# Kernel tuning notes

Measured on AMD Instinct MI355X. Metric: run time of the kernel, lower is better.

Reference implementation:

```python
import jax, jax.numpy as jnp
import numpy as np

N_PTS = 100000
C_IN, C_OUT, K = 16, 32, 3
B, D, H, W = 2, 32, 128, 128


def setup_inputs() -> dict:
    key = jax.random.key(0)
    kf, kw, kb, kz, ky, kx = jax.random.split(key, 6)
    features = jax.random.normal(kf, (N_PTS, C_IN), dtype=jnp.float32)
    coords = jnp.stack([
        jax.random.randint(kb, (N_PTS,), 0, B),
        jax.random.randint(kz, (N_PTS,), 0, D),
        jax.random.randint(ky, (N_PTS,), 0, H),
        jax.random.randint(kx, (N_PTS,), 0, W),
    ], axis=1).astype(jnp.int32)
    weight = jax.random.normal(kw, (K ** 3, C_IN, C_OUT), dtype=jnp.float32) * 0.01
    bias = jnp.zeros((C_OUT,), dtype=jnp.float32)
    return {"features": features, "coords": coords, "weight": weight, "bias": bias,
            "batch_size": B, "d_sp": D, "h_sp": H, "w_sp": W}


def reference(features, coords, weight, bias, batch_size, d_sp, h_sp, w_sp):
    # Scatter sparse voxel features into dense grid (B, C_in, D, H, W).
    n, c_in = features.shape
    c_out = weight.shape[2]
    k = K
    b, z, y, x = coords[:, 0], coords[:, 1], coords[:, 2], coords[:, 3]
    dense = jnp.zeros((batch_size, c_in, d_sp, h_sp, w_sp), dtype=features.dtype)
    dense = dense.at[b, :, z, y, x].set(features)  # (N,) advanced idx -> rows of (N, C_in)
    # Conv3d: torch copies weight.view(C_out, C_in, k, k, k) -> OIDHW kernel.
    kernel = weight.reshape(c_out, c_in, k, k, k)
    out = jax.lax.conv_general_dilated(
        dense, kernel,
        window_strides=(1, 1, 1),
        padding=[(1, 1), (1, 1), (1, 1)],
        dimension_numbers=("NCDHW", "OIDHW", "NCDHW"))
    out = jax.nn.relu(out + bias[None, :, None, None, None])
    # Dense equivalent of the torch nonzero-gather (which has data-dependent
    # shape): return the full dense activated grid (B, C_out, D, H, W).
    return out
```

## Files before the change

### kernel.cpp

```cpp
#include <hip/hip_runtime.h>

#define CIN   16
#define COUT  32
#define BATCH 2
#define DSP   32
#define HSP   128
#define WSP   128
#define NVOX  (BATCH*DSP*HSP*WSP)

#define DP (DSP+2)
#define HP (HSP+2)
#define WP (WSP+2)
#define ZSTR (HP*WP)
#define NVOXP (BATCH*DP*HP*WP)
#define NDCH  (NVOXP*2)

#define TZ 4
#define TY 8
#define TX 32
#define PZ 6
#define PYY 10
#define PXX 34
#define PROW (PYY*PXX)
#define PVOX (PZ*PROW)
#define NCHUNK (2*PVOX)
#define NCHPAD 4096
#define NPAIR 14
#define NWREP ((NPAIR*2*64*8 + 255)/256)

typedef __bf16 bf16x8 __attribute__((ext_vector_type(8)));
typedef float  f32x4  __attribute__((ext_vector_type(4)));

__device__ __forceinline__ void load_lds16(const void* g, void* l) {
    __builtin_amdgcn_global_load_lds(
        (const __attribute__((address_space(1))) unsigned*)g,
        (__attribute__((address_space(3))) unsigned*)l, 16, 0, 0);
}

__global__ void k_prep(const int4* __restrict__ coords, int n, int nbDedup,
                       int* __restrict__ map,
                       const float* __restrict__ w, __bf16* __restrict__ wpack) {
    int bb = blockIdx.x;
    if (bb < nbDedup) {
        int p = bb * 256 + threadIdx.x;
        if (p >= n) return;
        int4 c = coords[p];
        int vox = ((c.x*DSP + c.y)*HSP + c.z)*WSP + c.w;
        atomicMax(&map[vox], p);
    } else {
        int i = (bb - nbDedup) * 256 + threadIdx.x;
        if (i >= NPAIR*2*64*8) return;
        int j = i & 7, l = (i>>3) & 63, h = (i>>9) & 1, p = i >> 10;
        int tap = 2*p + ((l>>4)>>1);
        int co  = h*16 + (l & 15);
        int ci  = ((l>>4)&1)*8 + j;
        float v = (tap < 27) ? w[(co*CIN + ci)*27 + tap] : 0.0f;
        wpack[i] = (__bf16)v;
    }
}

__global__ void k_fill(const int* __restrict__ map, const float* __restrict__ feat,
                       __bf16* __restrict__ dense) {
    int c = blockIdx.x * 256 + threadIdx.x;
    if (c >= NDCH) return;
    int v = c >> 1, h = c & 1;
    int bb = v / (DP*ZSTR);
    int r  = v - bb*(DP*ZSTR);
    int zp = r / ZSTR;  r -= zp*ZSTR;
    int yp = r / WP;
    int xp = r - yp*WP;
    bf16x8 val = { (__bf16)0.f,(__bf16)0.f,(__bf16)0.f,(__bf16)0.f,
                   (__bf16)0.f,(__bf16)0.f,(__bf16)0.f,(__bf16)0.f };
    if ((unsigned)(zp-1) < DSP && (unsigned)(yp-1) < HSP && (unsigned)(xp-1) < WSP) {
        int vox = ((bb*DSP + (zp-1))*HSP + (yp-1))*WSP + (xp-1);
        int p = map[vox];
        if (p >= 0) {
            const float4* fp = (const float4*)(feat + (size_t)p*CIN) + h*2;
            float4 f0 = fp[0], f1 = fp[1];
            val = bf16x8{ (__bf16)f0.x,(__bf16)f0.y,(__bf16)f0.z,(__bf16)f0.w,
                          (__bf16)f1.x,(__bf16)f1.y,(__bf16)f1.z,(__bf16)f1.w };
        }
    }
    *(bf16x8*)(dense + (size_t)v*CIN + h*8) = val;
}

__device__ __forceinline__ void stage_tile(const __bf16* __restrict__ gb,
                                           ushort* lbase, int wave, int lane) {
    #pragma unroll
    for (int it = 0; it < 8; ++it) {
        int j0 = wave*64 + it*512;
        int j  = j0 + lane;
        int jj = j < NCHUNK ? j : NCHUNK-1;
        int h  = (jj >= PVOX) ? 1 : 0;
        int v  = jj - h*PVOX;
        int pz = v / PROW;
        int rem = v - pz*PROW;
        int py = rem / PXX;
        int px = rem - py*PXX;
        load_lds16(gb + ((size_t)(pz*ZSTR + py*WP + px))*CIN + h*8,
                   (void*)(lbase + (size_t)j0*8));
    }
}

__global__ __launch_bounds__(512, 2) void k_conv(
    const __bf16* __restrict__ dense, const __bf16* __restrict__ wpack,
    const float* __restrict__ bias, float* __restrict__ out)
{
    __shared__ __align__(16) ushort patch[2][NCHPAD*8];

    int bid = blockIdx.x;
    int bs  = (bid & 7) * 32 + (bid >> 3);
    int tyi = bs & 15, tzi = (bs >> 4) & 7, b = bs >> 7;
    int z0 = tzi*TZ, y0 = tyi*TY;

    int tid  = threadIdx.x;
    int lane = tid & 63, wave = tid >> 6;
    int lx16  = lane & 15;
    int lhalf = (lane >> 4) & 1;
    int ltp   = (lane >> 4) >> 1;
    int zw    = wave >> 1;
    int yb    = (wave & 1) * 4;

    int voff[NPAIR];
    #pragma unroll
    for (int p = 0; p < NPAIR; ++p) {
        int tap = 2*p + ltp; if (tap > 26) tap = 26;
        int kd = tap/9, kh = (tap/3)%3, kw = tap%3;
        voff[p] = (kd*PYY + kh)*PXX + kw;
    }
    float bv0 = bias[lx16], bv1 = bias[16 + lx16];

    bf16x8 wf[NPAIR][2];
    #pragma unroll
    for (int p = 0; p < NPAIR; ++p)
        #pragma unroll
        for (int h = 0; h < 2; ++h)
            wf[p][h] = *(const bf16x8*)(wpack + (size_t)((p*2 + h)*64 + lane)*8);

    const __bf16* grow = dense + ((((size_t)b*DP + z0)*HP + y0)*WP)*CIN;

    stage_tile(grow, patch[0], wave, lane);

    #pragma unroll 1
    for (int t = 0; t < 4; ++t) {
        if (t < 3) stage_tile(grow + (size_t)(t+1)*TX*CIN, patch[(t+1)&1], wave, lane);
        if (t == 0)      asm volatile("s_waitcnt vmcnt(8)\ns_barrier"  ::: "memory");
        else if (t < 3)  asm volatile("s_waitcnt vmcnt(24)\ns_barrier" ::: "memory");
        else             asm volatile("s_waitcnt vmcnt(16)\ns_barrier" ::: "memory");
        __builtin_amdgcn_sched_barrier(0);

        f32x4 acc[8][2];
        #pragma unroll
        for (int gi = 0; gi < 8; ++gi) {
            acc[gi][0] = (f32x4){0.f,0.f,0.f,0.f};
            acc[gi][1] = (f32x4){0.f,0.f,0.f,0.f};
        }
        const ushort* pb = patch[t&1] +
            ((size_t)lhalf*PVOX + (zw*PYY + yb)*PXX + lx16)*8;
        #pragma unroll
        for (int p = 0; p < NPAIR; ++p) {
            const ushort* pa = pb + (size_t)voff[p]*8;
            #pragma unroll
            for (int gi = 0; gi < 8; ++gi) {
                bf16x8 a = *(const bf16x8*)(pa + ((gi>>1)*PXX + (gi&1)*16)*8);
                acc[gi][0] = __builtin_amdgcn_mfma_f32_16x16x32_bf16(a, wf[p][0], acc[gi][0], 0,0,0);
                acc[gi][1] = __builtin_amdgcn_mfma_f32_16x16x32_bf16(a, wf[p][1], acc[gi][1], 0,0,0);
            }
        }

        asm volatile("s_barrier" ::: "memory");
        __builtin_amdgcn_sched_barrier(0);

        #pragma unroll
        for (int gi = 0; gi < 8; ++gi) {
            int y = yb + (gi >> 1), xg = gi & 1;
            int gz = z0 + zw, gy = y0 + y;
            int gx = t*TX + xg*16 + ((lane >> 4) << 2);
            f32x4 o0, o1;
            o0[0] = fmaxf(acc[gi][0][0]+bv0, 0.f); o0[1] = fmaxf(acc[gi][0][1]+bv0, 0.f);
            o0[2] = fmaxf(acc[gi][0][2]+bv0, 0.f); o0[3] = fmaxf(acc[gi][0][3]+bv0, 0.f);
            o1[0] = fmaxf(acc[gi][1][0]+bv1, 0.f); o1[1] = fmaxf(acc[gi][1][1]+bv1, 0.f);
            o1[2] = fmaxf(acc[gi][1][2]+bv1, 0.f); o1[3] = fmaxf(acc[gi][1][3]+bv1, 0.f);
            size_t base0 = ((((size_t)b*COUT + lx16)*DSP + gz)*HSP + gy)*WSP + gx;
            size_t base1 = base0 + (size_t)16*DSP*HSP*WSP;
            *(f32x4*)(out + base0) = o0;
            *(f32x4*)(out + base1) = o1;
        }
    }
}

extern "C" void kernel_launch(void* const* d_in, const int* in_sizes, int n_in,
                              void* d_out, int out_size, void* d_ws, size_t ws_size,
                              hipStream_t stream) {
    const float* feat   = (const float*)d_in[0];
    const int4*  coords = (const int4*)d_in[1];
    const float* weight = (const float*)d_in[2];
    const float* bias   = (const float*)d_in[3];
    float* out = (float*)d_out;
    int n = in_sizes[0] / CIN;

    int*    map   = (int*)d_ws;
    __bf16* dense = (__bf16*)(map + NVOX);
    __bf16* wpack = dense + (size_t)NVOXP*CIN;

    hipMemsetAsync(map, 0xFF, (size_t)NVOX*sizeof(int), stream);

    int nb = (n + 255) / 256;
    k_prep<<<nb + NWREP, 256, 0, stream>>>(coords, n, nb, map, weight, wpack);
    k_fill<<<(NDCH + 255)/256, 256, 0, stream>>>(map, feat, dense);
    k_conv<<<256, 512, 0, stream>>>(dense, wpack, bias, out);
}
```

Baseline: 73.41 us.

## Switch conv to 16x16x16 MFMA with channel-quartered layout and z-register reuse

The dense grid is re-laid out as four channel-quarter planes of 4 bf16 each, and the conv uses 16x16x16 bf16 MFMAs per tap instead of tap-paired 16x16x32. Each wave now owns one y row across all 4 z slices. It loads 6 z-planes of patch data once per (kh,kw,xg) and reuses them across the kd taps, which cuts LDS reads. The trade-off is twice as many MFMA instructions, each doing half the work, plus 27 weight fragments held in registers and more complex fill-kernel indexing.

```diff
diff --git a/kernel.cpp b/kernel.cpp
--- a/kernel.cpp
+++ b/kernel.cpp
@@ -11,9 +11,8 @@
 #define DP (DSP+2)
 #define HP (HSP+2)
 #define WP (WSP+2)
-#define ZSTR (HP*WP)
 #define NVOXP (BATCH*DP*HP*WP)
-#define NDCH  (NVOXP*2)
+#define NDCH2 (BATCH*4*DP*HP*(WP/2))
 
 #define TZ 4
 #define TY 8
@@ -23,13 +22,26 @@
 #define PXX 34
 #define PROW (PYY*PXX)
 #define PVOX (PZ*PROW)
-#define NCHUNK (2*PVOX)
+#define QCH   (PVOX/2)
+#define QUSH  (PVOX*4)
+#define NCHUNK (4*QCH)
 #define NCHPAD 4096
-#define NPAIR 14
-#define NWREP ((NPAIR*2*64*8 + 255)/256)
-
-typedef __bf16 bf16x8 __attribute__((ext_vector_type(8)));
+#define NWREP ((27*2*64*4 + 255)/256)
+
+typedef __bf16 bf16x4 __attribute__((ext_vector_type(4)));
+typedef short  s16x4  __attribute__((ext_vector_type(4)));
 typedef float  f32x4  __attribute__((ext_vector_type(4)));
+
+#if defined(__HIP_DEVICE_COMPILE__)
+  #if __has_builtin(__builtin_amdgcn_mfma_f32_16x16x16bf16_1k)
+    #define MFMA16(A,B,C) __builtin_amdgcn_mfma_f32_16x16x16bf16_1k((A),(B),(C),0,0,0)
+  #else
+    #define MFMA16(A,B,C) __builtin_amdgcn_mfma_f32_16x16x16_bf16( \
+        __builtin_bit_cast(bf16x4,(A)), __builtin_bit_cast(bf16x4,(B)), (C),0,0,0)
+  #endif
+#else
+  #define MFMA16(A,B,C) (C)
+#endif
 
 __device__ __forceinline__ void load_lds16(const void* g, void* l) {
     __builtin_amdgcn_global_load_lds(
@@ -49,39 +61,40 @@
         atomicMax(&map[vox], p);
     } else {
         int i = (bb - nbDedup) * 256 + threadIdx.x;
-        if (i >= NPAIR*2*64*8) return;
-        int j = i & 7, l = (i>>3) & 63, h = (i>>9) & 1, p = i >> 10;
-        int tap = 2*p + ((l>>4)>>1);
-        int co  = h*16 + (l & 15);
-        int ci  = ((l>>4)&1)*8 + j;
-        float v = (tap < 27) ? w[(co*CIN + ci)*27 + tap] : 0.0f;
-        wpack[i] = (__bf16)v;
+        if (i >= 27*2*64*4) return;
+        int j = i & 3, l = (i>>2) & 63, h = (i>>8) & 1, tap = i >> 9;
+        int co = h*16 + (l & 15);
+        int ci = (l>>4)*4 + j;
+        wpack[i] = (__bf16)w[(co*CIN + ci)*27 + tap];
     }
 }
 
 __global__ void k_fill(const int* __restrict__ map, const float* __restrict__ feat,
-                       __bf16* __restrict__ dense) {
+                       __bf16* __restrict__ dense2) {
     int c = blockIdx.x * 256 + threadIdx.x;
-    if (c >= NDCH) return;
-    int v = c >> 1, h = c & 1;
-    int bb = v / (DP*ZSTR);
-    int r  = v - bb*(DP*ZSTR);
-    int zp = r / ZSTR;  r -= zp*ZSTR;
-    int yp = r / WP;
-    int xp = r - yp*WP;
-    bf16x8 val = { (__bf16)0.f,(__bf16)0.f,(__bf16)0.f,(__bf16)0.f,
-                   (__bf16)0.f,(__bf16)0.f,(__bf16)0.f,(__bf16)0.f };
-    if ((unsigned)(zp-1) < DSP && (unsigned)(yp-1) < HSP && (unsigned)(xp-1) < WSP) {
-        int vox = ((bb*DSP + (zp-1))*HSP + (yp-1))*WSP + (xp-1);
-        int p = map[vox];
-        if (p >= 0) {
-            const float4* fp = (const float4*)(feat + (size_t)p*CIN) + h*2;
-            float4 f0 = fp[0], f1 = fp[1];
-            val = bf16x8{ (__bf16)f0.x,(__bf16)f0.y,(__bf16)f0.z,(__bf16)f0.w,
-                          (__bf16)f1.x,(__bf16)f1.y,(__bf16)f1.z,(__bf16)f1.w };
+    if (c >= NDCH2) return;
+    int px2 = c % 65;  int r1 = c / 65;
+    int yp  = r1 % HP; int r2 = r1 / HP;
+    int zp  = r2 % DP; int r3 = r2 / DP;
+    int q   = r3 & 3;  int b  = r3 >> 2;
+    ushort out8[8] = {0,0,0,0,0,0,0,0};
+    if ((unsigned)(zp-1) < DSP && (unsigned)(yp-1) < HSP) {
+        #pragma unroll
+        for (int s = 0; s < 2; ++s) {
+            int gx = 2*px2 + s - 1;
+            if ((unsigned)gx < WSP) {
+                int vox = ((b*DSP + (zp-1))*HSP + (yp-1))*WSP + gx;
+                int p = map[vox];
+                if (p >= 0) {
+                    float4 f = *(const float4*)(feat + (size_t)p*CIN + q*4);
+                    bf16x4 v = { (__bf16)f.x, (__bf16)f.y, (__bf16)f.z, (__bf16)f.w };
+                    *(bf16x4*)&out8[s*4] = v;
+                }
+            }
         }
     }
-    *(bf16x8*)(dense + (size_t)v*CIN + h*8) = val;
+    size_t idx = ((((size_t)(b*4 + q)*DP + zp)*HP + yp)*WP + 2*px2)*4;
+    *(uint4*)(dense2 + idx) = *(uint4*)out8;
 }
 
 __device__ __forceinline__ void stage_tile(const __bf16* __restrict__ gb,
@@ -91,19 +104,20 @@
         int j0 = wave*64 + it*512;
         int j  = j0 + lane;
         int jj = j < NCHUNK ? j : NCHUNK-1;
-        int h  = (jj >= PVOX) ? 1 : 0;
-        int v  = jj - h*PVOX;
+        int q  = jj / QCH;
+        int c2 = jj - q*QCH;
+        int v  = c2*2;
         int pz = v / PROW;
         int rem = v - pz*PROW;
         int py = rem / PXX;
         int px = rem - py*PXX;
-        load_lds16(gb + ((size_t)(pz*ZSTR + py*WP + px))*CIN + h*8,
+        load_lds16(gb + ((size_t)q*DP*HP*WP + (size_t)pz*HP*WP + (size_t)py*WP + px)*4,
                    (void*)(lbase + (size_t)j0*8));
     }
 }
 
 __global__ __launch_bounds__(512, 2) void k_conv(
-    const __bf16* __restrict__ dense, const __bf16* __restrict__ wpack,
+    const __bf16* __restrict__ dense2, const __bf16* __restrict__ wpack,
     const float* __restrict__ bias, float* __restrict__ out)
 {
     __shared__ __align__(16) ushort patch[2][NCHPAD*8];
@@ -115,72 +129,74 @@
 
     int tid  = threadIdx.x;
     int lane = tid & 63, wave = tid >> 6;
-    int lx16  = lane & 15;
-    int lhalf = (lane >> 4) & 1;
-    int ltp   = (lane >> 4) >> 1;
-    int zw    = wave >> 1;
-    int yb    = (wave & 1) * 4;
-
-    int voff[NPAIR];
+    int lx16 = lane & 15;
+    int lq   = lane >> 4;
+
+    float bv0 = bias[lx16], bv1 = bias[16 + lx16];
+
+    s16x4 wf[27][2];
     #pragma unroll
-    for (int p = 0; p < NPAIR; ++p) {
-        int tap = 2*p + ltp; if (tap > 26) tap = 26;
-        int kd = tap/9, kh = (tap/3)%3, kw = tap%3;
-        voff[p] = (kd*PYY + kh)*PXX + kw;
-    }
-    float bv0 = bias[lx16], bv1 = bias[16 + lx16];
-
-    bf16x8 wf[NPAIR][2];
-    #pragma unroll
-    for (int p = 0; p < NPAIR; ++p)
+    for (int tap = 0; tap < 27; ++tap)
         #pragma unroll
         for (int h = 0; h < 2; ++h)
-            wf[p][h] = *(const bf16x8*)(wpack + (size_t)((p*2 + h)*64 + lane)*8);
-
-    const __bf16* grow = dense + ((((size_t)b*DP + z0)*HP + y0)*WP)*CIN;
+            wf[tap][h] = *(const s16x4*)(wpack + (size_t)((tap*2 + h)*64 + lane)*4);
+
+    const __bf16* grow = dense2 + (((size_t)(b*4)*DP + z0)*HP + y0)*(size_t)WP*4;
 
     stage_tile(grow, patch[0], wave, lane);
 
     #pragma unroll 1
     for (int t = 0; t < 4; ++t) {
-        if (t < 3) stage_tile(grow + (size_t)(t+1)*TX*CIN, patch[(t+1)&1], wave, lane);
+        if (t < 3) stage_tile(grow + (size_t)(t+1)*TX*4, patch[(t+1)&1], wave, lane);
         if (t == 0)      asm volatile("s_waitcnt vmcnt(8)\ns_barrier"  ::: "memory");
         else if (t < 3)  asm volatile("s_waitcnt vmcnt(24)\ns_barrier" ::: "memory");
         else             asm volatile("s_waitcnt vmcnt(16)\ns_barrier" ::: "memory");
         __builtin_amdgcn_sched_barrier(0);
 
-        f32x4 acc[8][2];
-        #pragma unroll
-        for (int gi = 0; gi < 8; ++gi) {
-            acc[gi][0] = (f32x4){0.f,0.f,0.f,0.f};
-            acc[gi][1] = (f32x4){0.f,0.f,0.f,0.f};
-        }
-        const ushort* pb = patch[t&1] +
-            ((size_t)lhalf*PVOX + (zw*PYY + yb)*PXX + lx16)*8;
-        #pragma unroll
-        for (int p = 0; p < NPAIR; ++p) {
-            const ushort* pa = pb + (size_t)voff[p]*8;
+        f32x4 acc[4][2][2];
+        #pragma unroll
+        for (int z = 0; z < 4; ++z)
             #pragma unroll
-            for (int gi = 0; gi < 8; ++gi) {
-                bf16x8 a = *(const bf16x8*)(pa + ((gi>>1)*PXX + (gi&1)*16)*8);
-                acc[gi][0] = __builtin_amdgcn_mfma_f32_16x16x32_bf16(a, wf[p][0], acc[gi][0], 0,0,0);
-                acc[gi][1] = __builtin_amdgcn_mfma_f32_16x16x32_bf16(a, wf[p][1], acc[gi][1], 0,0,0);
+            for (int xg = 0; xg < 2; ++xg) {
+                acc[z][xg][0] = (f32x4){0.f,0.f,0.f,0.f};
+                acc[z][xg][1] = (f32x4){0.f,0.f,0.f,0.f};
             }
+        const ushort* pbase = patch[t&1] + lq*QUSH;
+        #pragma unroll
+        for (int kh = 0; kh < 3; ++kh)
+        #pragma unroll
+        for (int kw = 0; kw < 3; ++kw)
+        #pragma unroll
+        for (int xg = 0; xg < 2; ++xg) {
+            int vbase = (wave + kh)*PXX + xg*16 + kw + lx16;
+            s16x4 r[6];
+            #pragma unroll
+            for (int pz = 0; pz < 6; ++pz)
+                r[pz] = *(const s16x4*)(pbase + (size_t)(pz*PROW + vbase)*4);
+            #pragma unroll
+            for (int z = 0; z < 4; ++z)
+                #pragma unroll
+                for (int kd = 0; kd < 3; ++kd) {
+                    int tap = (kd*3 + kh)*3 + kw;
+                    acc[z][xg][0] = MFMA16(r[z+kd], wf[tap][0], acc[z][xg][0]);
+                    acc[z][xg][1] = MFMA16(r[z+kd], wf[tap][1], acc[z][xg][1]);
+                }
         }
 
         asm volatile("s_barrier" ::: "memory");
         __builtin_amdgcn_sched_barrier(0);
 
         #pragma unroll
-        for (int gi = 0; gi < 8; ++gi) {
-            int y = yb + (gi >> 1), xg = gi & 1;
-            int gz = z0 + zw, gy = y0 + y;
-            int gx = t*TX + xg*16 + ((lane >> 4) << 2);
+        for (int z = 0; z < 4; ++z)
+        #pragma unroll
+        for (int xg = 0; xg < 2; ++xg) {
+            int gz = z0 + z, gy = y0 + wave;
+            int gx = t*TX + xg*16 + (lq << 2);
             f32x4 o0, o1;
-            o0[0] = fmaxf(acc[gi][0][0]+bv0, 0.f); o0[1] = fmaxf(acc[gi][0][1]+bv0, 0.f);
-            o0[2] = fmaxf(acc[gi][0][2]+bv0, 0.f); o0[3] = fmaxf(acc[gi][0][3]+bv0, 0.f);
-            o1[0] = fmaxf(acc[gi][1][0]+bv1, 0.f); o1[1] = fmaxf(acc[gi][1][1]+bv1, 0.f);
-            o1[2] = fmaxf(acc[gi][1][2]+bv1, 0.f); o1[3] = fmaxf(acc[gi][1][3]+bv1, 0.f);
+            o0[0] = fmaxf(acc[z][xg][0][0]+bv0, 0.f); o0[1] = fmaxf(acc[z][xg][0][1]+bv0, 0.f);
+            o0[2] = fmaxf(acc[z][xg][0][2]+bv0, 0.f); o0[3] = fmaxf(acc[z][xg][0][3]+bv0, 0.f);
+            o1[0] = fmaxf(acc[z][xg][1][0]+bv1, 0.f); o1[1] = fmaxf(acc[z][xg][1][1]+bv1, 0.f);
+            o1[2] = fmaxf(acc[z][xg][1][2]+bv1, 0.f); o1[3] = fmaxf(acc[z][xg][1][3]+bv1, 0.f);
             size_t base0 = ((((size_t)b*COUT + lx16)*DSP + gz)*HSP + gy)*WSP + gx;
             size_t base1 = base0 + (size_t)16*DSP*HSP*WSP;
             *(f32x4*)(out + base0) = o0;
@@ -199,14 +215,14 @@
     float* out = (float*)d_out;
     int n = in_sizes[0] / CIN;
 
-    int*    map   = (int*)d_ws;
-    __bf16* dense = (__bf16*)(map + NVOX);
-    __bf16* wpack = dense + (size_t)NVOXP*CIN;
-
-    hipMemsetAsync(map, 0xFF, (size_t)NVOX*sizeof(int), stream);
+    int*    map    = (int*)d_ws;
+    __bf16* dense2 = (__bf16*)(map + NVOX);
+    __bf16* wpack  = dense2 + (size_t)NVOXP*CIN;
+
+    (void)hipMemsetAsync(map, 0xFF, (size_t)NVOX*sizeof(int), stream);
 
     int nb = (n + 255) / 256;
     k_prep<<<nb + NWREP, 256, 0, stream>>>(coords, n, nb, map, weight, wpack);
-    k_fill<<<(NDCH + 255)/256, 256, 0, stream>>>(map, feat, dense);
-    k_conv<<<256, 512, 0, stream>>>(dense, wpack, bias, out);
-}
+    k_fill<<<(NDCH2 + 255)/256, 256, 0, stream>>>(map, feat, dense2);
+    k_conv<<<256, 512, 0, stream>>>(dense2, wpack, bias, out);
+}
```

After: 84.52 us. +15.1%, slower.

## Shrink conv tiles, stage weights in LDS, double block count for occupancy

Applied to the files above, without the earlier changes.

The conv tile shrinks from 4x8x32 to 2x8x16 voxels and is swept along x in 8 steps instead of 4, with 512 blocks instead of 256. Weights now sit in LDS instead of a large register array, and the per-wave accumulator set drops from 8 output groups to 2, so launch bounds can ask for 4 blocks per CU. The aim is to cut register pressure and raise occupancy and parallelism so latency hides better. In exchange the z and x halo share of each staged patch grows, which adds redundant global loads, and every MFMA pair now needs extra LDS reads for its weight fragments. s_setprio is also raised around the MFMA loop.

```diff
diff --git a/kernel.cpp b/kernel.cpp
--- a/kernel.cpp
+++ b/kernel.cpp
@@ -11,22 +11,26 @@
 #define DP (DSP+2)
 #define HP (HSP+2)
 #define WP (WSP+2)
-#define ZSTR (HP*WP)
 #define NVOXP (BATCH*DP*HP*WP)
 #define NDCH  (NVOXP*2)
 
-#define TZ 4
+#define TZ 2
 #define TY 8
-#define TX 32
-#define PZ 6
+#define TX 16
+#define NTW 8
+#define PZ 4
 #define PYY 10
-#define PXX 34
+#define PXX 18
 #define PROW (PYY*PXX)
 #define PVOX (PZ*PROW)
 #define NCHUNK (2*PVOX)
-#define NCHPAD 4096
+#define SLICE  (NCHUNK/8)
 #define NPAIR 14
-#define NWREP ((NPAIR*2*64*8 + 255)/256)
+#define NWEL  (NPAIR*2*64*8)
+#define WCH   (NWEL/8)
+#define WSLICE (WCH/8)
+#define NWREP ((NWEL + 255)/256)
+#define NBLK  512
 
 typedef __bf16 bf16x8 __attribute__((ext_vector_type(8)));
 typedef float  f32x4  __attribute__((ext_vector_type(4)));
@@ -49,7 +53,7 @@
         atomicMax(&map[vox], p);
     } else {
         int i = (bb - nbDedup) * 256 + threadIdx.x;
-        if (i >= NPAIR*2*64*8) return;
+        if (i >= NWEL) return;
         int j = i & 7, l = (i>>3) & 63, h = (i>>9) & 1, p = i >> 10;
         int tap = 2*p + ((l>>4)>>1);
         int co  = h*16 + (l & 15);
@@ -64,9 +68,9 @@
     int c = blockIdx.x * 256 + threadIdx.x;
     if (c >= NDCH) return;
     int v = c >> 1, h = c & 1;
-    int bb = v / (DP*ZSTR);
-    int r  = v - bb*(DP*ZSTR);
-    int zp = r / ZSTR;  r -= zp*ZSTR;
+    int bb = v / (DP*HP*WP);
+    int r  = v - bb*(DP*HP*WP);
+    int zp = r / (HP*WP);  r -= zp*(HP*WP);
     int yp = r / WP;
     int xp = r - yp*WP;
     bf16x8 val = { (__bf16)0.f,(__bf16)0.f,(__bf16)0.f,(__bf16)0.f,
@@ -87,30 +91,32 @@
 __device__ __forceinline__ void stage_tile(const __bf16* __restrict__ gb,
                                            ushort* lbase, int wave, int lane) {
     #pragma unroll
-    for (int it = 0; it < 8; ++it) {
-        int j0 = wave*64 + it*512;
-        int j  = j0 + lane;
-        int jj = j < NCHUNK ? j : NCHUNK-1;
-        int h  = (jj >= PVOX) ? 1 : 0;
-        int v  = jj - h*PVOX;
-        int pz = v / PROW;
-        int rem = v - pz*PROW;
-        int py = rem / PXX;
-        int px = rem - py*PXX;
-        load_lds16(gb + ((size_t)(pz*ZSTR + py*WP + px))*CIN + h*8,
-                   (void*)(lbase + (size_t)j0*8));
-    }
-}
-
-__global__ __launch_bounds__(512, 2) void k_conv(
+    for (int it = 0; it < 3; ++it) {
+        int rel = it*64 + lane;
+        if (rel < SLICE) {
+            int j = wave*SLICE + rel;
+            int h = (j >= PVOX) ? 1 : 0;
+            int v = j - h*PVOX;
+            int pz = v / PROW;
+            int rm = v - pz*PROW;
+            int py = rm / PXX;
+            int px = rm - py*PXX;
+            load_lds16(gb + ((size_t)(pz*HP*WP + py*WP + px))*CIN + h*8,
+                       (void*)(lbase + (size_t)(wave*SLICE + it*64)*8));
+        }
+    }
+}
+
+__global__ __launch_bounds__(512, 4) void k_conv(
     const __bf16* __restrict__ dense, const __bf16* __restrict__ wpack,
     const float* __restrict__ bias, float* __restrict__ out)
 {
-    __shared__ __align__(16) ushort patch[2][NCHPAD*8];
+    __shared__ __align__(16) ushort patch[2][NCHUNK*8];
+    __shared__ __align__(16) ushort wlds[WCH*8];
 
     int bid = blockIdx.x;
-    int bs  = (bid & 7) * 32 + (bid >> 3);
-    int tyi = bs & 15, tzi = (bs >> 4) & 7, b = bs >> 7;
+    int bs  = (bid & 7) * (NBLK/8) + (bid >> 3);
+    int tyi = bs & 15, tzi = (bs >> 4) & 15, b = bs >> 8;
     int z0 = tzi*TZ, y0 = tyi*TY;
 
     int tid  = threadIdx.x;
@@ -118,8 +124,9 @@
     int lx16  = lane & 15;
     int lhalf = (lane >> 4) & 1;
     int ltp   = (lane >> 4) >> 1;
-    int zw    = wave >> 1;
-    int yb    = (wave & 1) * 4;
+    int lq    = lane >> 4;
+    int zw    = wave >> 2;
+    int ysub  = (wave & 3) * 2;
 
     int voff[NPAIR];
     #pragma unroll
@@ -130,52 +137,56 @@
     }
     float bv0 = bias[lx16], bv1 = bias[16 + lx16];
 
-    bf16x8 wf[NPAIR][2];
     #pragma unroll
-    for (int p = 0; p < NPAIR; ++p)
-        #pragma unroll
-        for (int h = 0; h < 2; ++h)
-            wf[p][h] = *(const bf16x8*)(wpack + (size_t)((p*2 + h)*64 + lane)*8);
-
-    const __bf16* grow = dense + ((((size_t)b*DP + z0)*HP + y0)*WP)*CIN;
-
-    stage_tile(grow, patch[0], wave, lane);
-
+    for (int it = 0; it < 4; ++it) {
+        int rel = it*64 + lane;
+        if (rel < WSLICE) {
+            int c0 = wave*WSLICE + it*64;
+            load_lds16(wpack + (size_t)(c0 + lane)*8, (void*)(wlds + (size_t)c0*8));
+        }
+    }
+    const __bf16* gbase = dense + ((((size_t)b*DP + z0)*HP + y0)*WP)*CIN;
+    stage_tile(gbase, patch[0], wave, lane);
+    asm volatile("s_waitcnt vmcnt(0)\ns_barrier" ::: "memory");
+    __builtin_amdgcn_sched_barrier(0);
+
+    int bufc = 0;
     #pragma unroll 1
-    for (int t = 0; t < 4; ++t) {
-        if (t < 3) stage_tile(grow + (size_t)(t+1)*TX*CIN, patch[(t+1)&1], wave, lane);
-        if (t == 0)      asm volatile("s_waitcnt vmcnt(8)\ns_barrier"  ::: "memory");
-        else if (t < 3)  asm volatile("s_waitcnt vmcnt(24)\ns_barrier" ::: "memory");
-        else             asm volatile("s_waitcnt vmcnt(16)\ns_barrier" ::: "memory");
+    for (int t = 0; t < NTW; ++t) {
+        if (t < NTW-1)
+            stage_tile(gbase + (size_t)(t+1)*TX*CIN, patch[bufc^1], wave, lane);
+        if (t == 0)          asm volatile("s_waitcnt vmcnt(3)\ns_barrier" ::: "memory");
+        else if (t < NTW-1)  asm volatile("s_waitcnt vmcnt(7)\ns_barrier" ::: "memory");
+        else                 asm volatile("s_waitcnt vmcnt(4)\ns_barrier" ::: "memory");
         __builtin_amdgcn_sched_barrier(0);
 
-        f32x4 acc[8][2];
-        #pragma unroll
-        for (int gi = 0; gi < 8; ++gi) {
-            acc[gi][0] = (f32x4){0.f,0.f,0.f,0.f};
-            acc[gi][1] = (f32x4){0.f,0.f,0.f,0.f};
-        }
-        const ushort* pb = patch[t&1] +
-            ((size_t)lhalf*PVOX + (zw*PYY + yb)*PXX + lx16)*8;
+        f32x4 acc[2][2];
+        acc[0][0] = (f32x4){0.f,0.f,0.f,0.f}; acc[0][1] = (f32x4){0.f,0.f,0.f,0.f};
+        acc[1][0] = (f32x4){0.f,0.f,0.f,0.f}; acc[1][1] = (f32x4){0.f,0.f,0.f,0.f};
+        const ushort* pb = patch[bufc] +
+            ((size_t)lhalf*PVOX + (zw*PYY + ysub)*PXX + lx16)*8;
+        __builtin_amdgcn_s_setprio(1);
         #pragma unroll
         for (int p = 0; p < NPAIR; ++p) {
+            bf16x8 w0 = *(const bf16x8*)(wlds + (size_t)((p*2+0)*64 + lane)*8);
+            bf16x8 w1 = *(const bf16x8*)(wlds + (size_t)((p*2+1)*64 + lane)*8);
             const ushort* pa = pb + (size_t)voff[p]*8;
             #pragma unroll
-            for (int gi = 0; gi < 8; ++gi) {
-                bf16x8 a = *(const bf16x8*)(pa + ((gi>>1)*PXX + (gi&1)*16)*8);
-                acc[gi][0] = __builtin_amdgcn_mfma_f32_16x16x32_bf16(a, wf[p][0], acc[gi][0], 0,0,0);
-                acc[gi][1] = __builtin_amdgcn_mfma_f32_16x16x32_bf16(a, wf[p][1], acc[gi][1], 0,0,0);
+            for (int gi = 0; gi < 2; ++gi) {
+                bf16x8 a = *(const bf16x8*)(pa + gi*(PXX*8));
+                acc[gi][0] = __builtin_amdgcn_mfma_f32_16x16x32_bf16(a, w0, acc[gi][0], 0,0,0);
+                acc[gi][1] = __builtin_amdgcn_mfma_f32_16x16x32_bf16(a, w1, acc[gi][1], 0,0,0);
             }
         }
+        __builtin_amdgcn_s_setprio(0);
 
         asm volatile("s_barrier" ::: "memory");
         __builtin_amdgcn_sched_barrier(0);
 
         #pragma unroll
-        for (int gi = 0; gi < 8; ++gi) {
-            int y = yb + (gi >> 1), xg = gi & 1;
-            int gz = z0 + zw, gy = y0 + y;
-            int gx = t*TX + xg*16 + ((lane >> 4) << 2);
+        for (int gi = 0; gi < 2; ++gi) {
+            int gz = z0 + zw, gy = y0 + ysub + gi;
+            int gx = t*TX + (lq << 2);
             f32x4 o0, o1;
             o0[0] = fmaxf(acc[gi][0][0]+bv0, 0.f); o0[1] = fmaxf(acc[gi][0][1]+bv0, 0.f);
             o0[2] = fmaxf(acc[gi][0][2]+bv0, 0.f); o0[3] = fmaxf(acc[gi][0][3]+bv0, 0.f);
@@ -186,6 +197,7 @@
             *(f32x4*)(out + base0) = o0;
             *(f32x4*)(out + base1) = o1;
         }
+        bufc ^= 1;
     }
 }
 
@@ -203,10 +215,10 @@
     __bf16* dense = (__bf16*)(map + NVOX);
     __bf16* wpack = dense + (size_t)NVOXP*CIN;
 
-    hipMemsetAsync(map, 0xFF, (size_t)NVOX*sizeof(int), stream);
+    (void)hipMemsetAsync(map, 0xFF, (size_t)NVOX*sizeof(int), stream);
 
     int nb = (n + 255) / 256;
     k_prep<<<nb + NWREP, 256, 0, stream>>>(coords, n, nb, map, weight, wpack);
     k_fill<<<(NDCH + 255)/256, 256, 0, stream>>>(map, feat, dense);
-    k_conv<<<256, 512, 0, stream>>>(dense, wpack, bias, out);
-}
+    k_conv<<<NBLK, 512, 0, stream>>>(dense, wpack, bias, out);
+}
```

Measured after the change: 68.29 us (median of 3 runs). -7.0%, faster.
